# Kernel optimization log

Measured on AMD Instinct MI355X. Metric: run time of the kernel, lower is better.

The kernel has to match this reference:

```python
import jax, jax.numpy as jnp
import numpy as np

N_TOKEN = 267735
D_EMBED = 1024
D_PROJ = 1024
DIV_VAL = 4
CUTOFFS = [20000, 40000, 200000, N_TOKEN]   # cutoffs + [n_token]
ENDS = [0] + CUTOFFS                         # cutoff_ends
N_CLUSTERS = len(CUTOFFS) - 1                # 3
HEAD_SIZE = CUTOFFS[0] + N_CLUSTERS          # 20003
N = 1024                                     # len*bsz


def setup_inputs() -> dict:
    key = jax.random.key(0)
    ks = jax.random.split(key, 16)
    d_embs = [D_EMBED // DIV_VAL ** i for i in range(4)]  # 1024,256,64,16
    sizes = [HEAD_SIZE] + [ENDS[i + 1] - ENDS[i] for i in range(1, 4)]  # 20003,20000,160000,67735
    s = 0.02
    inp = {
        'hidden': jax.random.normal(ks[0], (N, D_PROJ), dtype=jnp.float32),
        'target': jax.random.randint(ks[1], (N,), 0, N_TOKEN, dtype=jnp.int32),
    }
    for i in range(4):
        inp[f'w{i}'] = jax.random.normal(ks[2 + 3 * i], (sizes[i], d_embs[i]), dtype=jnp.float32) * s
        inp[f'b{i}'] = jnp.zeros((sizes[i],), dtype=jnp.float32)
        inp[f'p{i}'] = jax.random.normal(ks[3 + 3 * i], (D_PROJ, d_embs[i]), dtype=jnp.float32) * s
    return inp


def _logit(h, w, b, p):
    # F.linear(hidden, proj.t()) -> h @ p ; F.linear(., weight, bias) -> @ w.T + b
    return (h @ p) @ w.T + b


def reference(hidden, target, w0, b0, p0, w1, b1, p1, w2, b2, p2, w3, b3, p3):
    head_lp = jax.nn.log_softmax(_logit(hidden, w0, b0, p0), axis=1)  # [N, HEAD_SIZE]
    tails = [(w1, b1, p1), (w2, b2, p2), (w3, b3, p3)]
    lps = []
    # shortlist cluster: gather target logprob directly from head
    t0 = jnp.clip(target, 0, CUTOFFS[0] - 1)
    lps.append(jnp.take_along_axis(head_lp, t0[:, None], axis=1)[:, 0])
    # tail clusters: small projected matmul + log_softmax + gather, combined with cluster logprob head_lp[:, -i]
    for i in range(1, 4):
        l, r = ENDS[i], ENDS[i + 1]
        ti = jnp.clip(target - l, 0, r - l - 1)
        tail_lp = jax.nn.log_softmax(_logit(hidden, *tails[i - 1]), axis=1)  # [N, r-l]
        lps.append(head_lp[:, -i] + jnp.take_along_axis(tail_lp, ti[:, None], axis=1)[:, 0])
    masks = [(target >= ENDS[i]) & (target < ENDS[i + 1]) for i in range(4)]
    logprob = jnp.select(masks, lps)
    return -logprob  # [N] per-token NLL, original order (keep_order=True)
```

## Files before the change

### kernel.cpp

```cpp
#include <hip/hip_runtime.h>
#include <hip/hip_bf16.h>
#include <math.h>

#define NTOK 1024
#define DPROJ 1024
#define PSTRIDE 1376
#define HEADS 20003

typedef __attribute__((ext_vector_type(8))) short bf16x8;
typedef __attribute__((ext_vector_type(4))) float f32x4;
typedef long long i64;

__device__ __forceinline__ short f2bf(float f) {
    unsigned u = __float_as_uint(f);
    u += 0x7fffu + ((u >> 16) & 1u);
    return (short)(u >> 16);
}

__device__ __forceinline__ unsigned pk4fp8(float a, float b, float c, float d) {
    unsigned v = __builtin_amdgcn_cvt_pk_fp8_f32(a, b, 0, false);
    v = __builtin_amdgcn_cvt_pk_fp8_f32(c, d, v, true);
    return v;
}
__device__ __forceinline__ unsigned char fp8_1(float a) {
    return (unsigned char)(__builtin_amdgcn_cvt_pk_fp8_f32(a, a, 0, false) & 0xff);
}

__global__ __launch_bounds__(256) void prep(const float* __restrict__ hidden,
                                            const float* __restrict__ p0,
                                            const float* __restrict__ p1,
                                            const float* __restrict__ p2,
                                            const float* __restrict__ p3,
                                            short* __restrict__ hbP,
                                            short* __restrict__ pTbP0,
                                            short* __restrict__ pTbP1,
                                            short* __restrict__ pTbP2,
                                            short* __restrict__ pTbP3) {
    __shared__ float tile[64][65];
    int bid = blockIdx.x, tid = threadIdx.x;
    if (bid < 64) {
        int tt = bid;
        #pragma unroll
        for (int q = 0; q < 8; ++q) {
            int fi = q * 256 + tid;
            int l = fi & 63;
            int row = tt * 16 + (l & 15);
            int kb = (fi >> 6) * 32 + (l >> 4) * 8;
            const float* hp = hidden + row * 1024 + kb;
            float4 x = *(const float4*)hp;
            float4 y = *(const float4*)(hp + 4);
            bf16x8 o;
            o[0]=f2bf(x.x); o[1]=f2bf(x.y); o[2]=f2bf(x.z); o[3]=f2bf(x.w);
            o[4]=f2bf(y.x); o[5]=f2bf(y.y); o[6]=f2bf(y.z); o[7]=f2bf(y.w);
            *(bf16x8*)(hbP + (size_t)tt * 16384 + fi * 8) = o;
        }
        return;
    }
    int lb = bid - 64;
    const float* p; short* dst; int d, kt, jb;
    if (lb < 256)      { p = p0; dst = pTbP0; d = 1024; kt = lb >> 4; jb = lb & 15; }
    else if (lb < 320) { lb -= 256; p = p1; dst = pTbP1; d = 256; kt = lb >> 2; jb = lb & 3; }
    else if (lb < 336) { lb -= 320; p = p2; dst = pTbP2; d = 64;  kt = lb; jb = 0; }
    else               { lb -= 336; p = p3; dst = pTbP3; d = 16;  kt = lb; jb = 0; }
    int k0 = kt * 64, j0 = jb * 64;
    int tx = tid & 63, ty = tid >> 6;
    #pragma unroll
    for (int rr = 0; rr < 16; ++rr) {
        int k = k0 + ty * 16 + rr;
        int j = j0 + tx;
        if (j < d) tile[ty * 16 + rr][tx] = p[k * d + j];
    }
    __syncthreads();
    int ch = tid >> 5;
    int jtl = ch >> 1, ksl = ch & 1;
    int jt = jb * 4 + jtl;
    if (jt * 16 < d) {
        #pragma unroll
        for (int li = 0; li < 2; ++li) {
            int l = (tid & 31) + li * 32;
            int jl = jtl * 16 + (l & 15);
            int kl = ksl * 32 + (l >> 4) * 8;
            bf16x8 o;
            #pragma unroll
            for (int e = 0; e < 8; ++e) o[e] = f2bf(tile[kl + e][jl]);
            *(bf16x8*)(dst + ((size_t)jt * 32 + kt * 2 + ksl) * 512 + l * 8) = o;
        }
    }
}

__global__ __launch_bounds__(256) void proj(const short* __restrict__ hbP,
                                            const short* __restrict__ pTbP0,
                                            const short* __restrict__ pTbP1,
                                            const short* __restrict__ pTbP2,
                                            const short* __restrict__ pTbP3,
                                            float* __restrict__ projf,
                                            unsigned char* __restrict__ pk0,
                                            unsigned char* __restrict__ pk1,
                                            unsigned char* __restrict__ pk2,
                                            unsigned char* __restrict__ pk3) {
    __shared__ float spackf[16][72];
    __shared__ unsigned char sp8[1024];
    int tt = blockIdx.x, jbG = blockIdx.y, tid = threadIdx.x;
    const short* pB; unsigned char* pkc; int d, KSp, coloff, jb;
    if (jbG < 16)      { pB = pTbP0; pkc = pk0; d = 1024; KSp = 32; coloff = 0;    jb = jbG; }
    else if (jbG < 20) { pB = pTbP1; pkc = pk1; d = 256;  KSp = 8;  coloff = 1024; jb = jbG - 16; }
    else if (jbG == 20){ pB = pTbP2; pkc = pk2; d = 64;   KSp = 2;  coloff = 1280; jb = 0; }
    else               { pB = pTbP3; pkc = pk3; d = 16;   KSp = 1;  coloff = 1344; jb = 0; }
    int w = tid >> 6, lane = tid & 63;
    int l16 = lane & 15, quad = lane >> 4;
    int jt = jb * 4 + w;
    if (jt * 16 < d) {
        const short* ap = hbP + ((size_t)tt * 32) * 512 + lane * 8;
        const short* bp = pB  + ((size_t)jt * 32) * 512 + lane * 8;
        f32x4 x0 = {0,0,0,0}, x1 = {0,0,0,0};
        #pragma unroll
        for (int ks = 0; ks < 16; ++ks) {
            bf16x8 a0 = *(const bf16x8*)(ap + ks * 512);
            bf16x8 b0 = *(const bf16x8*)(bp + ks * 512);
            bf16x8 a1 = *(const bf16x8*)(ap + (ks + 16) * 512);
            bf16x8 b1 = *(const bf16x8*)(bp + (ks + 16) * 512);
            x0 = __builtin_amdgcn_mfma_f32_16x16x32_bf16(a0, b0, x0, 0, 0, 0);
            x1 = __builtin_amdgcn_mfma_f32_16x16x32_bf16(a1, b1, x1, 0, 0, 0);
        }
        f32x4 acc = x0 + x1;
        int kk = w * 16 + l16;
        #pragma unroll
        for (int r = 0; r < 4; ++r) {
            int tok = quad * 4 + r;
            spackf[tok][kk] = acc[r];
            sp8[(kk >> 5) * 512 + ((kk & 31) >> 3) * 128 + tok * 8 + (kk & 7)] = fp8_1(acc[r]);
        }
    }
    __syncthreads();
    int j0g = jb * 64;
    int dcols = min(64, d - j0g);
    {
        int row = tid >> 4, cb = (tid & 15) * 4;
        if (cb < dcols) {
            float4 v = *(const float4*)&spackf[row][cb];
            *(float4*)&projf[(tt * 16 + row) * PSTRIDE + coloff + j0g + cb] = v;
        }
    }
    {
        int nbytes = 16 * dcols;
        if (tid * 4 < nbytes) {
            unsigned char* gdst = pkc + ((size_t)tt * KSp + (j0g >> 5)) * 512;
            *(unsigned*)(gdst + tid * 4) = *(const unsigned*)(sp8 + tid * 4);
        }
    }
}

template <int KS, int VT>
__device__ __forceinline__ void lse_cluster(const float* __restrict__ w,
                                            const float* __restrict__ bias,
                                            const unsigned char* __restrict__ pkc,
                                            float* __restrict__ sumrowc,
                                            int V, int D, int bidLocal,
                                            float* bsum) {
    int tid = threadIdx.x;
    int wave = tid >> 6, lane = tid & 63;
    int quad = lane >> 4, l16 = lane & 15;
    int v0 = bidLocal * (64 * VT) + wave * (16 * VT);

    for (int i = tid; i < NTOK; i += 256) bsum[i] = 0.f;
    __syncthreads();

    i64 areg[VT][KS];
    float bb[VT][4];
    #pragma unroll
    for (int vt = 0; vt < VT; ++vt) {
        int va = v0 + vt * 16 + l16;
        #pragma unroll
        for (int ks = 0; ks < KS; ++ks) {
            int k = ks * 32 + quad * 8;
            if (va < V && k < D) {
                const float* wp = w + (long)va * D + k;
                float4 x = *(const float4*)(wp);
                float4 y = *(const float4*)(wp + 4);
                unsigned lo = pk4fp8(x.x, x.y, x.z, x.w);
                unsigned hi = pk4fp8(y.x, y.y, y.z, y.w);
                areg[vt][ks] = (i64)(((unsigned long long)hi << 32) | lo);
            } else {
                areg[vt][ks] = 0;
            }
        }
        #pragma unroll
        for (int r = 0; r < 4; ++r) {
            int vb = v0 + vt * 16 + quad * 4 + r;
            bb[vt][r] = (vb < V) ? bias[vb] : -1e30f;
        }
    }

    for (int tt = 0; tt < 64; ++tt) {
        const i64* bp = (const i64*)(pkc + (size_t)tt * KS * 512);
        i64 b[KS];
        #pragma unroll
        for (int ks = 0; ks < KS; ++ks) b[ks] = bp[ks * 64 + lane];
        float e = 0.f;
        #pragma unroll
        for (int vt = 0; vt < VT; ++vt) {
            f32x4 acc;
            if constexpr (KS >= 8) {
                f32x4 x0 = {0,0,0,0}, x1 = {0,0,0,0};
                #pragma unroll
                for (int j = 0; j < KS / 2; ++j) {
                    x0 = __builtin_amdgcn_mfma_f32_16x16x32_fp8_fp8(areg[vt][j], b[j], x0, 0, 0, 0);
                    x1 = __builtin_amdgcn_mfma_f32_16x16x32_fp8_fp8(areg[vt][KS/2 + j], b[KS/2 + j], x1, 0, 0, 0);
                }
                acc = x0 + x1;
            } else {
                f32x4 x0 = {0,0,0,0};
                #pragma unroll
                for (int j = 0; j < KS; ++j)
                    x0 = __builtin_amdgcn_mfma_f32_16x16x32_fp8_fp8(areg[vt][j], b[j], x0, 0, 0, 0);
                acc = x0;
            }
            e += __expf(acc[0] + bb[vt][0]) + __expf(acc[1] + bb[vt][1]) +
                 __expf(acc[2] + bb[vt][2]) + __expf(acc[3] + bb[vt][3]);
        }
        e += __shfl_xor(e, 16, 64);
        e += __shfl_xor(e, 32, 64);
        if (lane < 16) atomicAdd(&bsum[tt * 16 + lane], e);
    }
    __syncthreads();
    for (int i = tid; i < NTOK; i += 256)
        atomicAdd(&sumrowc[i], bsum[i]);
}

#define NB0 157
#define NB1 79
#define NB2 625
#define NB3 265

__global__ __launch_bounds__(256) void lse_all(const float* __restrict__ w0, const float* __restrict__ b0,
                                               const float* __restrict__ w1, const float* __restrict__ b1,
                                               const float* __restrict__ w2, const float* __restrict__ b2,
                                               const float* __restrict__ w3, const float* __restrict__ b3,
                                               const unsigned char* __restrict__ pk0,
                                               const unsigned char* __restrict__ pk1,
                                               const unsigned char* __restrict__ pk2,
                                               const unsigned char* __restrict__ pk3,
                                               float* __restrict__ sums) {
    __shared__ float bsum[NTOK];
    int bid = blockIdx.x;
    if (bid < NB0) {
        lse_cluster<32, 2>(w0, b0, pk0, sums,            HEADS,  1024, bid, bsum);
    } else if (bid < NB0 + NB1) {
        lse_cluster<8, 4>(w1, b1, pk1, sums + NTOK,      20000,  256,  bid - NB0, bsum);
    } else if (bid < NB0 + NB1 + NB2) {
        lse_cluster<2, 4>(w2, b2, pk2, sums + 2 * NTOK,  160000, 64,   bid - NB0 - NB1, bsum);
    } else {
        lse_cluster<1, 4>(w3, b3, pk3, sums + 3 * NTOK,  67735,  16,   bid - NB0 - NB1 - NB2, bsum);
    }
}

__global__ __launch_bounds__(256) void finalize(const int* __restrict__ target,
                                                const float* __restrict__ projf,
                                                const float* __restrict__ sums,
                                                const float* __restrict__ w0, const float* __restrict__ b0,
                                                const float* __restrict__ w1, const float* __restrict__ b1,
                                                const float* __restrict__ w2, const float* __restrict__ b2,
                                                const float* __restrict__ w3, const float* __restrict__ b3,
                                                float* __restrict__ out) {
    int wave = threadIdx.x >> 6, lane = threadIdx.x & 63;
    int row = blockIdx.x * 4 + wave;
    int t = target[row];
    int c = (t < 20000) ? 0 : (t < 40000) ? 1 : (t < 200000) ? 2 : 3;
    int col0 = (c == 0) ? t : (HEADS - c);
    const float* pr = projf + row * PSTRIDE;

    float s = 0.f;
    for (int k = lane; k < DPROJ; k += 64) s += pr[k] * w0[col0 * DPROJ + k];
    #pragma unroll
    for (int off = 32; off; off >>= 1) s += __shfl_xor(s, off, 64);
    float hl = s + b0[col0];
    float lse0 = __logf(sums[row]);

    float res;
    if (c == 0) {
        res = lse0 - hl;
    } else {
        const float* wc; const float* bc; int d, coloff, l;
        if (c == 1)      { wc = w1; bc = b1; d = 256; coloff = 1024; l = 20000; }
        else if (c == 2) { wc = w2; bc = b2; d = 64;  coloff = 1280; l = 40000; }
        else             { wc = w3; bc = b3; d = 16;  coloff = 1344; l = 200000; }
        int tc = t - l;
        float s2 = 0.f;
        for (int k = lane; k < d; k += 64) s2 += pr[coloff + k] * wc[tc * d + k];
        #pragma unroll
        for (int off = 32; off; off >>= 1) s2 += __shfl_xor(s2, off, 64);
        float tl = s2 + bc[tc];
        float lsec = __logf(sums[c * NTOK + row]);
        res = lse0 - hl + lsec - tl;
    }
    if (lane == 0) out[row] = res;
}


extern "C" void kernel_launch(void* const* d_in, const int* in_sizes, int n_in,
                              void* d_out, int out_size, void* d_ws, size_t ws_size,
                              hipStream_t stream) {
    const float* hidden = (const float*)d_in[0];
    const int*   target = (const int*)d_in[1];
    const float* w0 = (const float*)d_in[2];
    const float* b0 = (const float*)d_in[3];
    const float* p0 = (const float*)d_in[4];
    const float* w1 = (const float*)d_in[5];
    const float* b1 = (const float*)d_in[6];
    const float* p1 = (const float*)d_in[7];
    const float* w2 = (const float*)d_in[8];
    const float* b2 = (const float*)d_in[9];
    const float* p2 = (const float*)d_in[10];
    const float* w3 = (const float*)d_in[11];
    const float* b3 = (const float*)d_in[12];
    const float* p3 = (const float*)d_in[13];

    short* base = (short*)d_ws;
    short* hbP   = base;
    short* pTbP0 = base + 1048576;
    short* pTbP1 = base + 2097152;
    short* pTbP2 = base + 2359296;
    short* pTbP3 = base + 2424832;
    float* projf = (float*)((char*)d_ws + 4882432);
    unsigned char* pk0 = (unsigned char*)d_ws + 10518528;
    unsigned char* pk1 = pk0 + 1048576;
    unsigned char* pk2 = pk1 + 262144;
    unsigned char* pk3 = pk2 + 65536;
    float* sums  = (float*)pTbP0;

    prep<<<416, 256, 0, stream>>>(hidden, p0, p1, p2, p3, hbP, pTbP0, pTbP1, pTbP2, pTbP3);
    hipMemsetAsync(pk3, 0, 32768, stream);
    proj<<<dim3(64, 22), 256, 0, stream>>>(hbP, pTbP0, pTbP1, pTbP2, pTbP3,
                                           projf, pk0, pk1, pk2, pk3);
    hipMemsetAsync(sums, 0, 4 * NTOK * sizeof(float), stream);
    lse_all<<<NB0 + NB1 + NB2 + NB3, 256, 0, stream>>>(w0, b0, w1, b1, w2, b2, w3, b3,
                                                       pk0, pk1, pk2, pk3, sums);
    finalize<<<256, 256, 0, stream>>>(target, projf, sums,
                                      w0, b0, w1, b1, w2, b2, w3, b3, (float*)d_out);
}
```

Before: 371.4 us.

## Stage head fp8 tiles through LDS, use exp2 scaling, fold memsets into prep

The head cluster now double-buffers the packed fp8 projection tiles into shared memory with async global-to-LDS loads, and uses four independent MFMA accumulators. Tail clusters software-prefetch the next tile's B fragments into registers. Weights are prescaled by 4*log2e and projections by 0.25 so exp2f replaces expf and fp8 range is better used. The two hipMemsetAsync calls become extra blocks in the prep kernel, and launch bounds request 2 blocks per CU. The cost is 32KB of extra LDS per block, a barrier per tile in the head path, and a change in fp8 rounding behaviour.

```diff
diff --git a/kernel.cpp b/kernel.cpp
--- a/kernel.cpp
+++ b/kernel.cpp
@@ -6,6 +6,10 @@
 #define DPROJ 1024
 #define PSTRIDE 1376
 #define HEADS 20003
+#define LOG2E 1.4426950408889634f
+#define LN2   0.6931471805599453f
+#define WSCALE (4.0f * LOG2E)
+#define PSCALE 0.25f
 
 typedef __attribute__((ext_vector_type(8))) short bf16x8;
 typedef __attribute__((ext_vector_type(4))) float f32x4;
@@ -16,7 +20,6 @@
     u += 0x7fffu + ((u >> 16) & 1u);
     return (short)(u >> 16);
 }
-
 __device__ __forceinline__ unsigned pk4fp8(float a, float b, float c, float d) {
     unsigned v = __builtin_amdgcn_cvt_pk_fp8_f32(a, b, 0, false);
     v = __builtin_amdgcn_cvt_pk_fp8_f32(c, d, v, true);
@@ -24,6 +27,13 @@
 }
 __device__ __forceinline__ unsigned char fp8_1(float a) {
     return (unsigned char)(__builtin_amdgcn_cvt_pk_fp8_f32(a, a, 0, false) & 0xff);
+}
+__device__ __forceinline__ i64 wfrag(const float* wp) {
+    float4 x = *(const float4*)(wp);
+    float4 y = *(const float4*)(wp + 4);
+    unsigned lo = pk4fp8(x.x * WSCALE, x.y * WSCALE, x.z * WSCALE, x.w * WSCALE);
+    unsigned hi = pk4fp8(y.x * WSCALE, y.y * WSCALE, y.z * WSCALE, y.w * WSCALE);
+    return (i64)(((unsigned long long)hi << 32) | lo);
 }
 
 __global__ __launch_bounds__(256) void prep(const float* __restrict__ hidden,
@@ -35,9 +45,23 @@
                                             short* __restrict__ pTbP0,
                                             short* __restrict__ pTbP1,
                                             short* __restrict__ pTbP2,
-                                            short* __restrict__ pTbP3) {
+                                            short* __restrict__ pTbP3,
+                                            float* __restrict__ sums,
+                                            unsigned char* __restrict__ pk3) {
     __shared__ float tile[64][65];
     int bid = blockIdx.x, tid = threadIdx.x;
+    if (bid == 416) {
+        float4 z = {0.f, 0.f, 0.f, 0.f};
+        #pragma unroll
+        for (int i = 0; i < 4; ++i) *((float4*)sums + i * 256 + tid) = z;
+        return;
+    }
+    if (bid == 417) {
+        int4 z = {0, 0, 0, 0};
+        #pragma unroll
+        for (int i = 0; i < 8; ++i) *((int4*)pk3 + i * 256 + tid) = z;
+        return;
+    }
     if (bid < 64) {
         int tt = bid;
         #pragma unroll
@@ -128,7 +152,7 @@
         for (int r = 0; r < 4; ++r) {
             int tok = quad * 4 + r;
             spackf[tok][kk] = acc[r];
-            sp8[(kk >> 5) * 512 + ((kk & 31) >> 3) * 128 + tok * 8 + (kk & 7)] = fp8_1(acc[r]);
+            sp8[(kk >> 5) * 512 + ((kk & 31) >> 3) * 128 + tok * 8 + (kk & 7)] = fp8_1(acc[r] * PSCALE);
         }
     }
     __syncthreads();
@@ -150,81 +174,146 @@
     }
 }
 
-template <int KS, int VT>
-__device__ __forceinline__ void lse_cluster(const float* __restrict__ w,
-                                            const float* __restrict__ bias,
-                                            const unsigned char* __restrict__ pkc,
-                                            float* __restrict__ sumrowc,
-                                            int V, int D, int bidLocal,
-                                            float* bsum) {
+__device__ __forceinline__ void stage16k(const unsigned char* g, unsigned char* l,
+                                         int wave, int lane) {
+    const unsigned char* gs = g + wave * 4096 + lane * 16;
+    unsigned char* ls = l + wave * 4096;
+    #pragma unroll
+    for (int i = 0; i < 4; ++i)
+        __builtin_amdgcn_global_load_lds(
+            (const __attribute__((address_space(1))) unsigned*)(gs + i * 1024),
+            (__attribute__((address_space(3))) unsigned*)(ls + i * 1024), 16, 0, 0);
+}
+
+__device__ __forceinline__ void lse_head(const float* __restrict__ w,
+                                         const float* __restrict__ bias,
+                                         const unsigned char* __restrict__ pk,
+                                         float* __restrict__ sumrow, int bid,
+                                         unsigned char (*sbuf)[16384], float* bsum) {
     int tid = threadIdx.x;
     int wave = tid >> 6, lane = tid & 63;
     int quad = lane >> 4, l16 = lane & 15;
-    int v0 = bidLocal * (64 * VT) + wave * (16 * VT);
+    int v0 = bid * 128 + wave * 32;
 
     for (int i = tid; i < NTOK; i += 256) bsum[i] = 0.f;
-    __syncthreads();
-
-    i64 areg[VT][KS];
-    float bb[VT][4];
-    #pragma unroll
-    for (int vt = 0; vt < VT; ++vt) {
+
+    i64 areg[2][32];
+    float bb[2][4];
+    #pragma unroll
+    for (int vt = 0; vt < 2; ++vt) {
         int va = v0 + vt * 16 + l16;
         #pragma unroll
-        for (int ks = 0; ks < KS; ++ks) {
-            int k = ks * 32 + quad * 8;
-            if (va < V && k < D) {
-                const float* wp = w + (long)va * D + k;
-                float4 x = *(const float4*)(wp);
-                float4 y = *(const float4*)(wp + 4);
-                unsigned lo = pk4fp8(x.x, x.y, x.z, x.w);
-                unsigned hi = pk4fp8(y.x, y.y, y.z, y.w);
-                areg[vt][ks] = (i64)(((unsigned long long)hi << 32) | lo);
-            } else {
-                areg[vt][ks] = 0;
-            }
+        for (int ks = 0; ks < 32; ++ks) {
+            areg[vt][ks] = (va < HEADS) ? wfrag(w + (long)va * 1024 + ks * 32 + quad * 8) : 0;
         }
         #pragma unroll
         for (int r = 0; r < 4; ++r) {
             int vb = v0 + vt * 16 + quad * 4 + r;
-            bb[vt][r] = (vb < V) ? bias[vb] : -1e30f;
-        }
-    }
-
+            bb[vt][r] = (vb < HEADS) ? bias[vb] * LOG2E : -1e30f;
+        }
+    }
+
+    stage16k(pk, sbuf[0], wave, lane);
+    __syncthreads();
     for (int tt = 0; tt < 64; ++tt) {
-        const i64* bp = (const i64*)(pkc + (size_t)tt * KS * 512);
-        i64 b[KS];
-        #pragma unroll
-        for (int ks = 0; ks < KS; ++ks) b[ks] = bp[ks * 64 + lane];
-        float e = 0.f;
-        #pragma unroll
-        for (int vt = 0; vt < VT; ++vt) {
-            f32x4 acc;
-            if constexpr (KS >= 8) {
-                f32x4 x0 = {0,0,0,0}, x1 = {0,0,0,0};
-                #pragma unroll
-                for (int j = 0; j < KS / 2; ++j) {
-                    x0 = __builtin_amdgcn_mfma_f32_16x16x32_fp8_fp8(areg[vt][j], b[j], x0, 0, 0, 0);
-                    x1 = __builtin_amdgcn_mfma_f32_16x16x32_fp8_fp8(areg[vt][KS/2 + j], b[KS/2 + j], x1, 0, 0, 0);
-                }
-                acc = x0 + x1;
-            } else {
-                f32x4 x0 = {0,0,0,0};
-                #pragma unroll
-                for (int j = 0; j < KS; ++j)
-                    x0 = __builtin_amdgcn_mfma_f32_16x16x32_fp8_fp8(areg[vt][j], b[j], x0, 0, 0, 0);
-                acc = x0;
-            }
-            e += __expf(acc[0] + bb[vt][0]) + __expf(acc[1] + bb[vt][1]) +
-                 __expf(acc[2] + bb[vt][2]) + __expf(acc[3] + bb[vt][3]);
-        }
+        if (tt < 63) stage16k(pk + (size_t)(tt + 1) * 16384, sbuf[(tt + 1) & 1], wave, lane);
+        const unsigned char* sb = sbuf[tt & 1];
+        f32x4 x0 = {0,0,0,0}, x1 = x0, x2 = x0, x3 = x0;
+        #pragma unroll
+        for (int j = 0; j < 16; ++j) {
+            i64 b0 = *(const i64*)(sb + j * 512 + lane * 8);
+            i64 b1 = *(const i64*)(sb + (j + 16) * 512 + lane * 8);
+            x0 = __builtin_amdgcn_mfma_f32_16x16x32_fp8_fp8(areg[0][j],      b0, x0, 0, 0, 0);
+            x1 = __builtin_amdgcn_mfma_f32_16x16x32_fp8_fp8(areg[0][j + 16], b1, x1, 0, 0, 0);
+            x2 = __builtin_amdgcn_mfma_f32_16x16x32_fp8_fp8(areg[1][j],      b0, x2, 0, 0, 0);
+            x3 = __builtin_amdgcn_mfma_f32_16x16x32_fp8_fp8(areg[1][j + 16], b1, x3, 0, 0, 0);
+        }
+        f32x4 a0 = x0 + x1, a1 = x2 + x3;
+        float e0 = exp2f(a0[0] + bb[0][0]) + exp2f(a0[2] + bb[0][2]) +
+                   exp2f(a1[0] + bb[1][0]) + exp2f(a1[2] + bb[1][2]);
+        float e1 = exp2f(a0[1] + bb[0][1]) + exp2f(a0[3] + bb[0][3]) +
+                   exp2f(a1[1] + bb[1][1]) + exp2f(a1[3] + bb[1][3]);
+        float e = e0 + e1;
         e += __shfl_xor(e, 16, 64);
         e += __shfl_xor(e, 32, 64);
         if (lane < 16) atomicAdd(&bsum[tt * 16 + lane], e);
+        __syncthreads();
+    }
+    for (int i = tid; i < NTOK; i += 256)
+        atomicAdd(&sumrow[i], bsum[i]);
+}
+
+template <int KS, int VT>
+__device__ __forceinline__ void lse_tail(const float* __restrict__ w,
+                                         const float* __restrict__ bias,
+                                         const unsigned char* __restrict__ pk,
+                                         float* __restrict__ sumrow,
+                                         int V, int D, int bid, float* bsum) {
+    int tid = threadIdx.x;
+    int wave = tid >> 6, lane = tid & 63;
+    int quad = lane >> 4, l16 = lane & 15;
+    int v0 = bid * (64 * VT) + wave * (16 * VT);
+
+    for (int i = tid; i < NTOK; i += 256) bsum[i] = 0.f;
+    __syncthreads();
+
+    i64 areg[VT][KS];
+    float bb[VT][4];
+    #pragma unroll
+    for (int vt = 0; vt < VT; ++vt) {
+        int va = v0 + vt * 16 + l16;
+        #pragma unroll
+        for (int ks = 0; ks < KS; ++ks) {
+            int k = ks * 32 + quad * 8;
+            areg[vt][ks] = (va < V && k < D) ? wfrag(w + (long)va * D + k) : 0;
+        }
+        #pragma unroll
+        for (int r = 0; r < 4; ++r) {
+            int vb = v0 + vt * 16 + quad * 4 + r;
+            bb[vt][r] = (vb < V) ? bias[vb] * LOG2E : -1e30f;
+        }
+    }
+
+    const i64* base = (const i64*)pk;
+    i64 bn[KS];
+    #pragma unroll
+    for (int k = 0; k < KS; ++k) bn[k] = base[k * 64 + lane];
+    for (int tt = 0; tt < 64; ++tt) {
+        i64 bc[KS];
+        #pragma unroll
+        for (int k = 0; k < KS; ++k) bc[k] = bn[k];
+        if (tt < 63) {
+            const i64* nb = base + (size_t)(tt + 1) * KS * 64;
+            #pragma unroll
+            for (int k = 0; k < KS; ++k) bn[k] = nb[k * 64 + lane];
+        }
+        float e0 = 0.f, e1 = 0.f;
+        #pragma unroll
+        for (int vt = 0; vt < VT; ++vt) {
+            f32x4 acc;
+            if constexpr (KS >= 2) {
+                f32x4 y0 = {0,0,0,0}, y1 = {0,0,0,0};
+                #pragma unroll
+                for (int j = 0; j < KS / 2; ++j) {
+                    y0 = __builtin_amdgcn_mfma_f32_16x16x32_fp8_fp8(areg[vt][j], bc[j], y0, 0, 0, 0);
+                    y1 = __builtin_amdgcn_mfma_f32_16x16x32_fp8_fp8(areg[vt][KS/2 + j], bc[KS/2 + j], y1, 0, 0, 0);
+                }
+                acc = y0 + y1;
+            } else {
+                f32x4 y0 = {0,0,0,0};
+                acc = __builtin_amdgcn_mfma_f32_16x16x32_fp8_fp8(areg[vt][0], bc[0], y0, 0, 0, 0);
+            }
+            e0 += exp2f(acc[0] + bb[vt][0]) + exp2f(acc[2] + bb[vt][2]);
+            e1 += exp2f(acc[1] + bb[vt][1]) + exp2f(acc[3] + bb[vt][3]);
+        }
+        float e = e0 + e1;
+        e += __shfl_xor(e, 16, 64);
+        e += __shfl_xor(e, 32, 64);
+        if (lane < 16) atomicAdd(&bsum[tt * 16 + lane], e);
     }
     __syncthreads();
     for (int i = tid; i < NTOK; i += 256)
-        atomicAdd(&sumrowc[i], bsum[i]);
+        atomicAdd(&sumrow[i], bsum[i]);
 }
 
 #define NB0 157
@@ -232,25 +321,26 @@
 #define NB2 625
 #define NB3 265
 
-__global__ __launch_bounds__(256) void lse_all(const float* __restrict__ w0, const float* __restrict__ b0,
-                                               const float* __restrict__ w1, const float* __restrict__ b1,
-                                               const float* __restrict__ w2, const float* __restrict__ b2,
-                                               const float* __restrict__ w3, const float* __restrict__ b3,
-                                               const unsigned char* __restrict__ pk0,
-                                               const unsigned char* __restrict__ pk1,
-                                               const unsigned char* __restrict__ pk2,
-                                               const unsigned char* __restrict__ pk3,
-                                               float* __restrict__ sums) {
+__global__ __launch_bounds__(256, 2) void lse_all(const float* __restrict__ w0, const float* __restrict__ b0,
+                                                  const float* __restrict__ w1, const float* __restrict__ b1,
+                                                  const float* __restrict__ w2, const float* __restrict__ b2,
+                                                  const float* __restrict__ w3, const float* __restrict__ b3,
+                                                  const unsigned char* __restrict__ pk0,
+                                                  const unsigned char* __restrict__ pk1,
+                                                  const unsigned char* __restrict__ pk2,
+                                                  const unsigned char* __restrict__ pk3,
+                                                  float* __restrict__ sums) {
+    __shared__ unsigned char sbuf[2][16384];
     __shared__ float bsum[NTOK];
     int bid = blockIdx.x;
     if (bid < NB0) {
-        lse_cluster<32, 2>(w0, b0, pk0, sums,            HEADS,  1024, bid, bsum);
+        lse_head(w0, b0, pk0, sums, bid, sbuf, bsum);
     } else if (bid < NB0 + NB1) {
-        lse_cluster<8, 4>(w1, b1, pk1, sums + NTOK,      20000,  256,  bid - NB0, bsum);
+        lse_tail<8, 4>(w1, b1, pk1, sums + NTOK,     20000,  256, bid - NB0, bsum);
     } else if (bid < NB0 + NB1 + NB2) {
-        lse_cluster<2, 4>(w2, b2, pk2, sums + 2 * NTOK,  160000, 64,   bid - NB0 - NB1, bsum);
+        lse_tail<2, 4>(w2, b2, pk2, sums + 2 * NTOK, 160000, 64,  bid - NB0 - NB1, bsum);
     } else {
-        lse_cluster<1, 4>(w3, b3, pk3, sums + 3 * NTOK,  67735,  16,   bid - NB0 - NB1 - NB2, bsum);
+        lse_tail<1, 4>(w3, b3, pk3, sums + 3 * NTOK, 67735,  16,  bid - NB0 - NB1 - NB2, bsum);
     }
 }
 
@@ -274,7 +364,7 @@
     #pragma unroll
     for (int off = 32; off; off >>= 1) s += __shfl_xor(s, off, 64);
     float hl = s + b0[col0];
-    float lse0 = __logf(sums[row]);
+    float lse0 = __log2f(sums[row]) * LN2;
 
     float res;
     if (c == 0) {
@@ -290,7 +380,7 @@
         #pragma unroll
         for (int off = 32; off; off >>= 1) s2 += __shfl_xor(s2, off, 64);
         float tl = s2 + bc[tc];
-        float lsec = __logf(sums[c * NTOK + row]);
+        float lsec = __log2f(sums[c * NTOK + row]) * LN2;
         res = lse0 - hl + lsec - tl;
     }
     if (lane == 0) out[row] = res;
@@ -326,13 +416,12 @@
     unsigned char* pk1 = pk0 + 1048576;
     unsigned char* pk2 = pk1 + 262144;
     unsigned char* pk3 = pk2 + 65536;
-    float* sums  = (float*)pTbP0;
-
-    prep<<<416, 256, 0, stream>>>(hidden, p0, p1, p2, p3, hbP, pTbP0, pTbP1, pTbP2, pTbP3);
-    hipMemsetAsync(pk3, 0, 32768, stream);
+    float* sums  = (float*)((char*)d_ws + 11927552);
+
+    prep<<<418, 256, 0, stream>>>(hidden, p0, p1, p2, p3,
+                                  hbP, pTbP0, pTbP1, pTbP2, pTbP3, sums, pk3);
     proj<<<dim3(64, 22), 256, 0, stream>>>(hbP, pTbP0, pTbP1, pTbP2, pTbP3,
                                            projf, pk0, pk1, pk2, pk3);
-    hipMemsetAsync(sums, 0, 4 * NTOK * sizeof(float), stream);
     lse_all<<<NB0 + NB1 + NB2 + NB3, 256, 0, stream>>>(w0, b0, w1, b1, w2, b2, w3, b3,
                                                        pk0, pk1, pk2, pk3, sums);
     finalize<<<256, 256, 0, stream>>>(target, projf, sums,
```

Result: faster. 350.0 us (-5.8%).
